# Kernel optimization log

Hardware: AMD Instinct MI355X
Metric: run time of the kernel (lower is better)

## Reference

```python
import jax, jax.numpy as jnp
import numpy as np

B, S, T = 1024, 1024, 32
TAGS = ["O"] + [p + f"T{i}" for i in range(1, 16) for p in ("B-", "I-")] + ["B-T16"]
MASKED = -1.0e4


def _init_params(key):
    bound = float(np.sqrt(6.0 / T))
    k1, k2, k3 = jax.random.split(key, 3)
    start = np.array(jax.random.uniform(k1, (T,), minval=-bound, maxval=bound))
    trans = np.array(jax.random.uniform(k2, (T, T), minval=-bound, maxval=bound))
    end = np.array(jax.random.uniform(k3, (T,), minval=-bound, maxval=bound))
    # structural BIO masking, as in _initialize_parameters
    for i, src in enumerate(TAGS):
        if src.startswith("I-"):
            start[i] = MASKED
        for j, tgt in enumerate(TAGS):
            if (src.startswith("B-") or src.startswith("I-")) and tgt.startswith("I-") and src[2:] != tgt[2:]:
                trans[i, j] = MASKED
            elif src == "O" and tgt.startswith("I-"):
                trans[i, j] = MASKED
    return jnp.asarray(start, jnp.float32), jnp.asarray(trans, jnp.float32), jnp.asarray(end, jnp.float32)


def setup_inputs() -> dict:
    key = jax.random.key(0)
    k_em, k_tag, k_len, k_par = jax.random.split(key, 4)
    emissions = jax.random.normal(k_em, (B, S, T), dtype=jnp.float32)
    tags = jax.random.randint(k_tag, (B, S), 0, T, dtype=jnp.int64) if jax.config.jax_enable_x64 else jax.random.randint(k_tag, (B, S), 0, T).astype(jnp.int32)
    lengths = jax.random.randint(k_len, (B,), S // 4, S + 1)
    mask = jnp.arange(S)[None, :] < lengths[:, None]  # prefix mask, bool [B, S]
    start_transitions, transitions, end_transitions = _init_params(k_par)
    return {
        "emissions": emissions,
        "tags": tags,
        "mask": mask,
        "start_transitions": start_transitions,
        "transitions": transitions,
        "end_transitions": end_transitions,
    }


def reference(emissions, tags, mask, start_transitions, transitions, end_transitions):
    b, s, t = emissions.shape
    ar = jnp.arange(s)
    bidx = jnp.arange(b)
    head = jnp.min(jnp.where(mask, ar[None, :], s - 1), axis=1)  # [B]
    tail = jnp.max(ar[None, :] * mask, axis=1)                   # [B]
    nonempty = mask.sum(axis=1) != 0

    # condition[:, j-1] == (mask[:, j] and head != j), for j = 1..S-1
    cond = mask[:, 1:] & (head[:, None] != ar[None, 1:])  # [B, S-1]

    # ---- numerator (gold path score): additive, fully vectorized ----
    head_tags = tags[bidx, head]
    tail_tags = tags[bidx, tail]
    em_tag = jnp.take_along_axis(emissions, tags[:, :, None], axis=2)[:, :, 0]  # [B, S]
    trans_step = transitions[tags[:, :-1], tags[:, 1:]]                          # [B, S-1]
    numerator = (start_transitions[head_tags]
                 + em_tag[bidx, head]
                 + jnp.sum(jnp.where(cond, trans_step + em_tag[:, 1:], 0.0), axis=1)
                 + end_transitions[tail_tags])
    numerator = jnp.where(nonempty, numerator, 0.0)

    # ---- denominator (log partition): scan over time ----
    score0 = start_transitions[None, :] + emissions[bidx, head]  # [B, T]

    def step(score, xs):
        em_j, cond_j = xs  # [B, T], [B]
        nxt = jax.nn.logsumexp(score[:, :, None] + transitions[None, :, :] + em_j[:, None, :], axis=1)
        return jnp.where(cond_j[:, None], nxt, score), None

    em_seq = jnp.moveaxis(emissions[:, 1:, :], 1, 0)  # [S-1, B, T]
    cond_seq = jnp.moveaxis(cond, 1, 0)               # [S-1, B]
    score_final, _ = jax.lax.scan(step, score0, (em_seq, cond_seq))
    denominator = jax.nn.logsumexp(score_final + end_transitions[None, :], axis=1)
    denominator = jnp.where(nonempty, denominator, 0.0)

    # ---- token_mean reduction ----
    llh = denominator - numerator
    labels = mask.sum(axis=1).astype(emissions.dtype)
    eps = 1e-6
    return jnp.sum(llh / (labels + eps)) / (jnp.sum(labels != 0).astype(emissions.dtype) + eps)
```

## Files before the change

kernel.cpp:

```cpp
#include <hip/hip_runtime.h>
#include <cstdint>

static constexpr int S = 1024;
static constexpr int T = 32;
static constexpr float L2E  = 1.4426950408889634f;
static constexpr float LN2f = 0.6931471805599453f;

typedef __attribute__((ext_vector_type(8)))  short  short8;
typedef __attribute__((ext_vector_type(16))) float  float16;

union Frag { unsigned u[4]; short8 s; };

__global__ void crf_zero(float* ws) {
  ws[0] = 0.0f; ws[1] = 0.0f; ((unsigned*)ws)[2] = 0u;
}

__device__ __forceinline__ float bcast_lane(float v, int k) {
  return __uint_as_float((unsigned)__builtin_amdgcn_readlane((int)__float_as_uint(v), k));
}

__device__ __forceinline__ unsigned cvtpk(float lo, float hi) {
  unsigned r;
  asm("v_cvt_pk_bf16_f32 %0, %1, %2" : "=v"(r) : "v"(lo), "v"(hi));
  return r;
}

__device__ __forceinline__ void gload16(const float* src, float* dst) {
  __builtin_amdgcn_global_load_lds(
      (const __attribute__((address_space(1))) unsigned int*)(src),
      (__attribute__((address_space(3))) unsigned int*)(dst),
      16, 0, 0);
}

__device__ __forceinline__ int sig(int k) {
  int g2 = (k >> 2) & 3;
  if (g2 == 1) g2 = 2; else if (g2 == 2) g2 = 1;
  return (k & ~12) | (g2 << 2);
}

__global__ __launch_bounds__(512, 8) void crf_main(
    const float* __restrict__ em, const int* __restrict__ tags,
    const int* __restrict__ mask, const float* __restrict__ startT,
    const float* __restrict__ trans, const float* __restrict__ endT,
    float* __restrict__ ws, float* __restrict__ out, int B)
{
  __shared__ __align__(16) unsigned s_pool[8 * 544];
  __shared__ float s_trans[1024];
  __shared__ short s_tags[1024];
  __shared__ unsigned long long s_mb[17];
  __shared__ int   s_head, s_tail, s_cnt, s_K[8];
  __shared__ float s_num[8];

  const int tid = threadIdx.x;
  const int l   = tid & 63;
  const int wv  = tid >> 6;
  const int b   = blockIdx.x;
  const int n   = l & 31;
  const int h   = l >> 5;

  const float* emb   = em   + (size_t)b * S * T;
  const int*   maskb = mask + (size_t)b * S;
  const int*   tagsb = tags + (size_t)b * S;

  for (int i = tid; i < 1024; i += 512) {
    s_tags[i]  = (short)tagsb[i];
    s_trans[i] = trans[i];
  }
  {
    unsigned long long b0 = __ballot(maskb[wv * 128 + l] != 0);
    unsigned long long b1 = __ballot(maskb[wv * 128 + 64 + l] != 0);
    if (l == 0) { s_mb[2 * wv] = b0; s_mb[2 * wv + 1] = b1; }
    if (tid == 0) s_mb[16] = 0ull;
  }

  Frag Alo, Ahi;
  #pragma unroll
  for (int p = 0; p < 4; ++p) {
    int k0 = 8 * h + 2 * p;
    Alo.u[p] = cvtpk(exp2f(trans[sig(k0 + 0)      * T + n] * L2E),
                     exp2f(trans[sig(k0 + 1)      * T + n] * L2E));
    Ahi.u[p] = cvtpk(exp2f(trans[sig(16 + k0 + 0) * T + n] * L2E),
                     exp2f(trans[sig(16 + k0 + 1) * T + n] * L2E));
  }
  __syncthreads();

  if (wv == 0) {
    int first = 0x7fffffff, last = -1, pc = 0;
    if (l < 16) {
      unsigned long long w = s_mb[l];
      if (w) {
        first = 64 * l + (int)__builtin_ctzll(w);
        last  = 64 * l + 63 - (int)__builtin_clzll(w);
        pc    = (int)__builtin_popcountll(w);
      }
    }
    #pragma unroll
    for (int d = 1; d < 64; d <<= 1) {
      first = min(first, __shfl_xor(first, d));
      last  = max(last,  __shfl_xor(last,  d));
      pc   += __shfl_xor(pc, d);
    }
    if (l == 0) { s_head = first; s_tail = last; s_cnt = pc; }
  }
  __syncthreads();
  const int cnt  = s_cnt;
  const int head = (cnt > 0) ? s_head : 0;
  const int tail = (cnt > 0) ? s_tail : 0;

  const int span = tail - head;
  const int Lc   = (span + 7) >> 3;
  const int c0   = head + 1 + wv * Lc;
  const int c1   = min(c0 + Lc, tail + 1);

  float* bcur = (float*)s_pool + wv * 512;
  float* bnxt = bcur + 256;

  Frag Blo, Bhi;
  #pragma unroll
  for (int p = 0; p < 4; ++p) {
    int k0 = 8 * h + 2 * p;
    Blo.u[p] = ((sig(k0) == n)          ? 0x3F80u : 0u) |
               ((sig(k0 + 1) == n)      ? 0x3F800000u : 0u);
    Bhi.u[p] = ((sig(16 + k0) == n)     ? 0x3F80u : 0u) |
               ((sig(16 + k0 + 1) == n) ? 0x3F800000u : 0u);
  }
  int   Kacc  = 0;
  float numer = 0.0f;
  const float16 Zv = {0,0,0,0,0,0,0,0,0,0,0,0,0,0,0,0};

#define FOLD(JJ, RSC) do {                                                   \
    const float4* gw = (const float4*)(gp + (JJ) * 32);                      \
    float4 wa = gw[h], wb = gw[h + 2], wc = gw[h + 4], wd = gw[h + 6];       \
    float16 D = __builtin_amdgcn_mfma_f32_32x32x16_bf16(Alo.s, Blo.s, Zv, 0, 0, 0); \
    D = __builtin_amdgcn_mfma_f32_32x32x16_bf16(Ahi.s, Bhi.s, D, 0, 0, 0);   \
    D[0]  *= wa.x; D[1]  *= wa.y; D[2]  *= wa.z; D[3]  *= wa.w;              \
    D[4]  *= wb.x; D[5]  *= wb.y; D[6]  *= wb.z; D[7]  *= wb.w;              \
    D[8]  *= wc.x; D[9]  *= wc.y; D[10] *= wc.z; D[11] *= wc.w;              \
    D[12] *= wd.x; D[13] *= wd.y; D[14] *= wd.z; D[15] *= wd.w;              \
    if (RSC) {                                                               \
      float mx = fmaxf(fmaxf(fmaxf(D[0], D[1]), fmaxf(D[2], D[3])),          \
                       fmaxf(fmaxf(D[4], D[5]), fmaxf(D[6], D[7])));         \
      mx = fmaxf(mx, fmaxf(fmaxf(fmaxf(D[8], D[9]),  fmaxf(D[10], D[11])),   \
                           fmaxf(fmaxf(D[12], D[13]), fmaxf(D[14], D[15]))));\
      mx = fmaxf(mx, __shfl_xor(mx, 32));    \
      mx = __uint_as_float((unsigned)__builtin_amdgcn_readfirstlane(         \
               (int)__float_as_uint(mx)));                                   \
      int E = (int)((__float_as_uint(mx) >> 23) & 0xffu);                    \
      float sc = __uint_as_float((unsigned)(254 - E) << 23);                 \
      Kacc += E - 127;                                                       \
      _Pragma("unroll")                                                      \
      for (int q_ = 0; q_ < 16; ++q_) D[q_] *= sc;                           \
    }                                                                        \
    Blo.u[0] = cvtpk(D[0],  D[1]);  Blo.u[1] = cvtpk(D[2],  D[3]);           \
    Blo.u[2] = cvtpk(D[4],  D[5]);  Blo.u[3] = cvtpk(D[6],  D[7]);           \
    Bhi.u[0] = cvtpk(D[8],  D[9]);  Bhi.u[1] = cvtpk(D[10], D[11]);          \
    Bhi.u[2] = cvtpk(D[12], D[13]); Bhi.u[3] = cvtpk(D[14], D[15]);          \
  } while (0)

  if (c0 < c1) {
    const int base = min(c0, S - 8);
    gload16(emb + (size_t)base * T + 4 * l, bcur);
  }

  for (int j0 = c0; j0 < c1; j0 += 8) {
    const int ns   = min(8, c1 - j0);
    const int base = min(j0, S - 8);
    const int d    = j0 - base;

    asm volatile("s_waitcnt vmcnt(0)" ::: "memory");
    {
      float4 r = ((const float4*)bcur)[l];
      r.x = exp2f(r.x * L2E); r.y = exp2f(r.y * L2E);
      r.z = exp2f(r.z * L2E); r.w = exp2f(r.w * L2E);
      ((float4*)bcur)[l] = r;
    }

    if (j0 + 8 < c1) {
      const int nb = min(j0 + 8, S - 8);
      gload16(emb + (size_t)nb * T + 4 * l, bnxt);
    }

    const float* gp = bcur + d * 32;

    const int w = j0 >> 6, o = j0 & 63;
    unsigned long long bits = s_mb[w] >> o;
    if (o) bits |= s_mb[w + 1] << (64 - o);
    unsigned eff = (unsigned)(bits & 0xFFull) & (unsigned)((1u << ns) - 1u);

    if (l < ns && ((eff >> l) & 1u)) {
      int j  = j0 + l;
      int tg = (int)s_tags[j], tp = (int)s_tags[j - 1];
      float gval = gp[l * 32 + tg];
      numer += s_trans[tp * T + tg] + log2f(gval) * LN2f;
    }

    if (eff == 0xFFu) {
      #pragma unroll
      for (int jj = 0; jj < 8; ++jj) FOLD(jj, (jj == 7));
    } else {
      for (int jj = 0; jj < ns; ++jj)
        if ((eff >> jj) & 1u) FOLD(jj, true);
    }

    float* tmp = bcur; bcur = bnxt; bnxt = tmp;
  }
#undef FOLD

  __syncthreads();

  {
    unsigned* mw = s_pool + wv * 544;
    #pragma unroll
    for (int p = 0; p < 4; ++p) {
      mw[(sig(8 * h + 2 * p)      >> 1) * 34 + n] = Blo.u[p];
      mw[(sig(16 + 8 * h + 2 * p) >> 1) * 34 + n] = Bhi.u[p];
    }
  }
  #pragma unroll
  for (int d = 1; d < 64; d <<= 1) numer += __shfl_xor(numer, d);
  if (l == 0) { s_num[wv] = numer; s_K[wv] = Kacc; }
  __syncthreads();

  if (wv == 0) {
    const int t = n;
    const float em0 = emb[head * T + t];
    float sc0 = (startT[t] + em0) * L2E;
    float m0 = sc0;
    #pragma unroll
    for (int d = 1; d < 32; d <<= 1) m0 = fmaxf(m0, __shfl_xor(m0, d));
    float e = exp2f(sc0 - m0);
    float Mtot = m0;

    const unsigned sh = (t & 1) ? 0u : 16u;
    for (int c = 0; c < 8; ++c) {
      const unsigned* mw = s_pool + c * 544 + (t >> 1) * 34;
      float acc = 0.0f;
      #pragma unroll
      for (int q2 = 0; q2 < 16; ++q2) {
        uint2 w2 = *(const uint2*)(mw + 2 * q2);
        float vlo = __uint_as_float((w2.x << sh) & 0xFFFF0000u);
        float vhi = __uint_as_float((w2.y << sh) & 0xFFFF0000u);
        acc = fmaf(vlo, bcast_lane(e, 2 * q2), acc);
        acc = fmaf(vhi, bcast_lane(e, 2 * q2 + 1), acc);
      }
      e = acc;
      Mtot += (float)s_K[c];
      float mx = e;
      #pragma unroll
      for (int d = 1; d < 32; d <<= 1) mx = fmaxf(mx, __shfl_xor(mx, d));
      int E = (int)((__float_as_uint(mx) >> 23) & 0xffu);
      e *= __uint_as_float((unsigned)(254 - E) << 23);
      Mtot += (float)(E - 127);
    }

    float fv = e * exp2f(endT[t] * L2E);
    #pragma unroll
    for (int d = 1; d < 32; d <<= 1) fv += __shfl_xor(fv, d);
    float denom = (Mtot + log2f(fv)) * LN2f;

    if (l == 0) {
      if (cnt > 0) {
        float ntot = 0.0f;
        for (int wq = 0; wq < 8; ++wq) ntot += s_num[wq];
        int th = (int)s_tags[head], tt = (int)s_tags[tail];
        ntot += startT[th] + bcast_lane(em0, th) + endT[tt];
        atomicAdd(&ws[0], (denom - ntot) / ((float)cnt + 1e-6f));
        atomicAdd(&ws[1], 1.0f);
      }
      __threadfence();
      unsigned done = atomicAdd((unsigned*)ws + 2, 1u);
      if (done == (unsigned)(B - 1)) {
        __threadfence();
        out[0] = ws[0] / (ws[1] + 1e-6f);
      }
    }
  }
}

extern "C" void kernel_launch(void* const* d_in, const int* in_sizes, int n_in,
                              void* d_out, int out_size, void* d_ws, size_t ws_size,
                              hipStream_t stream) {
  const float* em     = (const float*)d_in[0];
  const int*   tags   = (const int*)d_in[1];
  const int*   mask   = (const int*)d_in[2];
  const float* startT = (const float*)d_in[3];
  const float* trans  = (const float*)d_in[4];
  const float* endT   = (const float*)d_in[5];
  float* out = (float*)d_out;
  float* ws  = (float*)d_ws;

  const int B = in_sizes[0] / (S * T);

  crf_zero<<<1, 1, 0, stream>>>(ws);
  crf_main<<<B, 512, 0, stream>>>(em, tags, mask, startT, trans, endT, ws, out, B);
}
```

Before: 261.9 us.

## Fold emission weights into the MFMA A operand and software-pipeline operand builds

After: 278.3 us. +6.3%, slower.

```diff
diff --git a/kernel.cpp b/kernel.cpp
--- a/kernel.cpp
+++ b/kernel.cpp
@@ -38,7 +38,7 @@
   return (k & ~12) | (g2 << 2);
 }
 
-__global__ __launch_bounds__(512, 8) void crf_main(
+__global__ __launch_bounds__(512, 6) void crf_main(
     const float* __restrict__ em, const int* __restrict__ tags,
     const int* __restrict__ mask, const float* __restrict__ startT,
     const float* __restrict__ trans, const float* __restrict__ endT,
@@ -73,14 +73,14 @@
     if (tid == 0) s_mb[16] = 0ull;
   }
 
-  Frag Alo, Ahi;
+  float bsl[8], bsh[8];
   #pragma unroll
   for (int p = 0; p < 4; ++p) {
     int k0 = 8 * h + 2 * p;
-    Alo.u[p] = cvtpk(exp2f(trans[sig(k0 + 0)      * T + n] * L2E),
-                     exp2f(trans[sig(k0 + 1)      * T + n] * L2E));
-    Ahi.u[p] = cvtpk(exp2f(trans[sig(16 + k0 + 0) * T + n] * L2E),
-                     exp2f(trans[sig(16 + k0 + 1) * T + n] * L2E));
+    bsl[2 * p + 0] = exp2f(trans[sig(k0 + 0)      * T + n] * L2E);
+    bsl[2 * p + 1] = exp2f(trans[sig(k0 + 1)      * T + n] * L2E);
+    bsh[2 * p + 0] = exp2f(trans[sig(16 + k0 + 0) * T + n] * L2E);
+    bsh[2 * p + 1] = exp2f(trans[sig(16 + k0 + 1) * T + n] * L2E);
   }
   __syncthreads();
 
@@ -128,15 +128,22 @@
   float numer = 0.0f;
   const float16 Zv = {0,0,0,0,0,0,0,0,0,0,0,0,0,0,0,0};
 
-#define FOLD(JJ, RSC) do {                                                   \
-    const float4* gw = (const float4*)(gp + (JJ) * 32);                      \
-    float4 wa = gw[h], wb = gw[h + 2], wc = gw[h + 4], wd = gw[h + 6];       \
-    float16 D = __builtin_amdgcn_mfma_f32_32x32x16_bf16(Alo.s, Blo.s, Zv, 0, 0, 0); \
-    D = __builtin_amdgcn_mfma_f32_32x32x16_bf16(Ahi.s, Bhi.s, D, 0, 0, 0);   \
-    D[0]  *= wa.x; D[1]  *= wa.y; D[2]  *= wa.z; D[3]  *= wa.w;              \
-    D[4]  *= wb.x; D[5]  *= wb.y; D[6]  *= wb.z; D[7]  *= wb.w;              \
-    D[8]  *= wc.x; D[9]  *= wc.y; D[10] *= wc.z; D[11] *= wc.w;              \
-    D[12] *= wd.x; D[13] *= wd.y; D[14] *= wd.z; D[15] *= wd.w;              \
+#define ABUILD(AL, AH, JJ) do {                                              \
+    float gn = exp2f(gp[(JJ) * 32 + n] * L2E);                               \
+    AL.u[0] = cvtpk(bsl[0] * gn, bsl[1] * gn);                               \
+    AL.u[1] = cvtpk(bsl[2] * gn, bsl[3] * gn);                               \
+    AL.u[2] = cvtpk(bsl[4] * gn, bsl[5] * gn);                               \
+    AL.u[3] = cvtpk(bsl[6] * gn, bsl[7] * gn);                               \
+    AH.u[0] = cvtpk(bsh[0] * gn, bsh[1] * gn);                               \
+    AH.u[1] = cvtpk(bsh[2] * gn, bsh[3] * gn);                               \
+    AH.u[2] = cvtpk(bsh[4] * gn, bsh[5] * gn);                               \
+    AH.u[3] = cvtpk(bsh[6] * gn, bsh[7] * gn);                               \
+  } while (0)
+
+#define FOLDP(AL, AH, NL, NH, JN, RSC) do {                                  \
+    float16 D = __builtin_amdgcn_mfma_f32_32x32x16_bf16(AL.s, Blo.s, Zv, 0, 0, 0); \
+    D = __builtin_amdgcn_mfma_f32_32x32x16_bf16(AH.s, Bhi.s, D, 0, 0, 0);    \
+    if ((JN) >= 0) ABUILD(NL, NH, JN);                                       \
     if (RSC) {                                                               \
       float mx = fmaxf(fmaxf(fmaxf(D[0], D[1]), fmaxf(D[2], D[3])),          \
                        fmaxf(fmaxf(D[4], D[5]), fmaxf(D[6], D[7])));         \
@@ -168,12 +175,6 @@
     const int d    = j0 - base;
 
     asm volatile("s_waitcnt vmcnt(0)" ::: "memory");
-    {
-      float4 r = ((const float4*)bcur)[l];
-      r.x = exp2f(r.x * L2E); r.y = exp2f(r.y * L2E);
-      r.z = exp2f(r.z * L2E); r.w = exp2f(r.w * L2E);
-      ((float4*)bcur)[l] = r;
-    }
 
     if (j0 + 8 < c1) {
       const int nb = min(j0 + 8, S - 8);
@@ -190,21 +191,33 @@
     if (l < ns && ((eff >> l) & 1u)) {
       int j  = j0 + l;
       int tg = (int)s_tags[j], tp = (int)s_tags[j - 1];
-      float gval = gp[l * 32 + tg];
-      numer += s_trans[tp * T + tg] + log2f(gval) * LN2f;
+      numer += s_trans[tp * T + tg] + gp[l * 32 + tg];
     }
 
     if (eff == 0xFFu) {
-      #pragma unroll
-      for (int jj = 0; jj < 8; ++jj) FOLD(jj, (jj == 7));
+      Frag Xl, Xh, Yl, Yh;
+      ABUILD(Xl, Xh, 0);
+      FOLDP(Xl, Xh, Yl, Yh, 1, false);
+      FOLDP(Yl, Yh, Xl, Xh, 2, false);
+      FOLDP(Xl, Xh, Yl, Yh, 3, false);
+      FOLDP(Yl, Yh, Xl, Xh, 4, false);
+      FOLDP(Xl, Xh, Yl, Yh, 5, false);
+      FOLDP(Yl, Yh, Xl, Xh, 6, false);
+      FOLDP(Xl, Xh, Yl, Yh, 7, false);
+      FOLDP(Yl, Yh, Xl, Xh, -1, true);
     } else {
       for (int jj = 0; jj < ns; ++jj)
-        if ((eff >> jj) & 1u) FOLD(jj, true);
+        if ((eff >> jj) & 1u) {
+          Frag Xl, Xh;
+          ABUILD(Xl, Xh, jj);
+          FOLDP(Xl, Xh, Xl, Xh, -1, true);
+        }
     }
 
     float* tmp = bcur; bcur = bnxt; bnxt = tmp;
   }
-#undef FOLD
+#undef FOLDP
+#undef ABUILD
 
   __syncthreads();
 
```
